# Kernel optimization log

Measured on AMD Instinct MI355X. Metric: run time of the kernel, lower is better.

## Reference

```python
import jax, jax.numpy as jnp
import numpy as np

NEG = -9e15
SLOPE = 0.1  # LeakyReLU negative_slope in the torch module

B, N, NFEAT = 4, 2048, 256
NHID, NHEADS, NOUT = 64, 8, 128


def setup_inputs() -> dict:
    key = jax.random.key(0)
    ks = jax.random.split(key, 8)
    x = jax.random.normal(ks[0], (B, N, NFEAT), dtype=jnp.float32)
    adj = jax.random.randint(ks[1], (B, N, N), 0, 2, dtype=jnp.int32)
    s = 0.1
    Wh = jax.random.normal(ks[2], (NHEADS, NFEAT, NHID), dtype=jnp.float32) * s
    ah = jax.random.normal(ks[3], (NHEADS, 2 * NHID), dtype=jnp.float32) * s
    bh = jax.random.normal(ks[4], (NHEADS, NHID), dtype=jnp.float32) * s
    Wo = jax.random.normal(ks[5], (NHID * NHEADS, NOUT), dtype=jnp.float32) * s
    ao = jax.random.normal(ks[6], (2 * NOUT,), dtype=jnp.float32) * s
    bo = jax.random.normal(ks[7], (NOUT,), dtype=jnp.float32) * s
    return {"x": x, "adj": adj, "Wh": Wh, "ah": ah, "bh": bh,
            "Wo": Wo, "ao": ao, "bo": bo}


def _leaky(v):
    return jnp.where(v >= 0, v, SLOPE * v)


def _gat_layer(x, adj, W, a, b):
    # x: [B,N,Fin], W: [Fin,F], a: [2F], b: [F]
    h = jnp.einsum('bnf,fo->bno', x, W)          # [B,N,F]
    F = W.shape[1]
    a1, a2 = a[:F], a[F:]
    s1 = h @ a1                                   # [B,N] (query / row term)
    s2 = h @ a2                                   # [B,N] (key / col term)
    e = _leaky(s1[:, :, None] + s2[:, None, :])   # [B,N,N], avoids a_input blowup
    e = jnp.where(adj > 0, e, NEG)
    att = jax.nn.softmax(e, axis=2)               # [B,N,N]
    h_prime = jnp.einsum('bnm,bmf->bnf', att, h) + b
    return jax.nn.elu(h_prime)


def reference(x, adj, Wh, ah, bh, Wo, ao, bo):
    # per-head layers, vmapped over the head axis of the stacked params
    heads = jax.vmap(lambda W, a, b: _gat_layer(x, adj, W, a, b))(Wh, ah, bh)
    # [H,B,N,F] -> concat heads along feature dim: [B,N,H*F]
    hcat = jnp.transpose(heads, (1, 2, 0, 3)).reshape(x.shape[0], x.shape[1], -1)
    out = _gat_layer(hcat, adj, Wo, ao, bo)
    return jax.nn.relu(out)
```

## Files before the change

kernel.cpp:

```cpp
#include <hip/hip_runtime.h>

constexpr int B_ = 4;
constexpr int N_ = 2048;
constexpr int NFEAT_ = 256;
constexpr int NHEADS_ = 8;
constexpr float SLOPE_ = 0.1f;
constexpr float L2E = 1.4426950408889634f;

typedef __attribute__((ext_vector_type(8))) __fp16 f16x8;
typedef __attribute__((ext_vector_type(2))) __fp16 f16x2;
typedef __attribute__((ext_vector_type(4))) float f32x4;

__device__ __forceinline__ f16x8 pack8(const float* v) {
  union { f16x2 h2[4]; f16x8 h8; } u;
  u.h2[0] = __builtin_amdgcn_cvt_pkrtz(v[0], v[1]);
  u.h2[1] = __builtin_amdgcn_cvt_pkrtz(v[2], v[3]);
  u.h2[2] = __builtin_amdgcn_cvt_pkrtz(v[4], v[5]);
  u.h2[3] = __builtin_amdgcn_cvt_pkrtz(v[6], v[7]);
  return u.h8;
}

__global__ __launch_bounds__(256) void k_packmask(
    const int* __restrict__ adj, unsigned short* __restrict__ mask2)
{
  const int l = threadIdx.x & 63;
  const size_t gw = ((size_t)blockIdx.x * 256 + threadIdx.x) >> 6;
  const int jt = (int)(gw & 31);
  const int ig16 = (int)((gw >> 5) & 127);
  const int b = (int)(gw >> 12);
  const int q = l >> 4, c15 = l & 15;

  const int* base = adj + ((size_t)b * N_ + ig16 * 16) * N_ + jt * 64 + l;
  unsigned int msk = 0;
  #pragma unroll
  for (int r = 0; r < 16; ++r) {
    int a = base[(size_t)r * N_];
    unsigned long long bal = __ballot(a > 0);
    unsigned int v = (unsigned int)((bal >> (q * 8)) & 0xffull)
                   | ((unsigned int)((bal >> (q * 8 + 32)) & 0xffull) << 8);
    if (r == c15) msk = v;
  }
  mask2[gw * 64 + l] = (unsigned short)msk;
}

__global__ __launch_bounds__(256) void k_rowmax(
    const float* __restrict__ src, float* __restrict__ dst)
{
  int row = blockIdx.x, t = threadIdx.x;
  const float* p = src + (size_t)row * N_;
  float m = -INFINITY;
  #pragma unroll
  for (int k = 0; k < N_ / 256; ++k) m = fmaxf(m, p[t + k * 256]);
  #pragma unroll
  for (int off = 1; off < 64; off <<= 1) m = fmaxf(m, __shfl_xor(m, off, 64));
  __shared__ float sm[4];
  if ((t & 63) == 0) sm[t >> 6] = m;
  __syncthreads();
  if (t == 0) dst[row] = fmaxf(fmaxf(sm[0], sm[1]), fmaxf(sm[2], sm[3]));
}

__global__ __launch_bounds__(256) void k_prepwh(
    const float* __restrict__ Wh, __fp16* __restrict__ WhB)
{
  int l = threadIdx.x & 63;
  int s = (int)((blockIdx.x * 256 + threadIdx.x) >> 6);
  int h = s >> 5, ks = (s >> 2) & 7, ft = s & 3;
  const float* src = Wh + ((size_t)h * 256 + ks * 32 + (l >> 4) * 8) * 64 + ft * 16 + (l & 15);
  float v[8];
  #pragma unroll
  for (int j = 0; j < 8; ++j) v[j] = src[(size_t)j * 64];
  *(f16x8*)(WhB + (size_t)s * 512 + l * 8) = pack8(v);
}

__global__ __launch_bounds__(256) void k_prepwo(
    const float* __restrict__ Wo, __fp16* __restrict__ WoB)
{
  int l = threadIdx.x & 63;
  int s = (int)((blockIdx.x * 256 + threadIdx.x) >> 6);
  int ks = s >> 3, ft = s & 7;
  const float* src = Wo + ((size_t)ks * 32 + (l >> 4) * 8) * 128 + ft * 16 + (l & 15);
  float v[8];
  #pragma unroll
  for (int j = 0; j < 8; ++j) v[j] = src[(size_t)j * 128];
  *(f16x8*)(WoB + (size_t)s * 512 + l * 8) = pack8(v);
}

__global__ __launch_bounds__(256, 4) void k_gemm1(
    const float* __restrict__ x, const __fp16* __restrict__ WhB,
    const float* __restrict__ ah,
    __fp16* __restrict__ hB1, float* __restrict__ s1h, float* __restrict__ s2h)
{
  constexpr int XP = 264;
  __shared__ __fp16 xs[16 * XP];
  __shared__ __fp16 hT[512 * 16];

  const int t = threadIdx.x;
  const int bid = blockIdx.x;
  const int b = bid >> 7;
  const int n0 = (bid & 127) * 16;

  {
    int r = t >> 4, k0 = (t & 15) * 16;
    const float* src = x + ((size_t)(b * N_) + n0 + r) * NFEAT_ + k0;
    float v0[8], v1[8];
    *(float4*)&v0[0] = *(const float4*)(src);
    *(float4*)&v0[4] = *(const float4*)(src + 4);
    *(float4*)&v1[0] = *(const float4*)(src + 8);
    *(float4*)&v1[4] = *(const float4*)(src + 12);
    *(f16x8*)&xs[r * XP + k0] = pack8(v0);
    *(f16x8*)&xs[r * XP + k0 + 8] = pack8(v1);
  }
  __syncthreads();

  const int w = t >> 6, l = t & 63;
  const int quad = l >> 4, c15 = l & 15;

  f32x4 acc[8];
  #pragma unroll
  for (int i = 0; i < 8; ++i) acc[i] = (f32x4){0.f, 0.f, 0.f, 0.f};

  for (int ks = 0; ks < 8; ++ks) {
    f16x8 af = *(const f16x8*)&xs[c15 * XP + ks * 32 + quad * 8];
    #pragma unroll
    for (int tt = 0; tt < 8; ++tt) {
      int hl = tt >> 2, ft = tt & 3;
      f16x8 bf = *(const f16x8*)(WhB +
          ((((size_t)(2 * w + hl) * 8 + ks) * 4 + ft) * 512) + l * 8);
      acc[tt] = __builtin_amdgcn_mfma_f32_16x16x32_f16(af, bf, acc[tt], 0, 0, 0);
    }
  }

  #pragma unroll
  for (int hl = 0; hl < 2; ++hl) {
    int head = 2 * w + hl;
    float a1v[4], a2v[4];
    #pragma unroll
    for (int ft = 0; ft < 4; ++ft) {
      a1v[ft] = ah[head * 128 + ft * 16 + c15] * L2E;
      a2v[ft] = ah[head * 128 + 64 + ft * 16 + c15] * L2E;
    }
    #pragma unroll
    for (int r = 0; r < 4; ++r) {
      float v1 = 0.f, v2 = 0.f;
      #pragma unroll
      for (int ft = 0; ft < 4; ++ft) {
        v1 = fmaf(acc[hl * 4 + ft][r], a1v[ft], v1);
        v2 = fmaf(acc[hl * 4 + ft][r], a2v[ft], v2);
      }
      #pragma unroll
      for (int off = 1; off < 16; off <<= 1) {
        v1 += __shfl_xor(v1, off, 64);
        v2 += __shfl_xor(v2, off, 64);
      }
      if (c15 == 0) {
        s1h[(size_t)(b * NHEADS_ + head) * N_ + n0 + quad * 4 + r] = v1;
        s2h[(size_t)(b * NHEADS_ + head) * N_ + n0 + quad * 4 + r] = v2;
      }
    }
  }

  #pragma unroll
  for (int tt = 0; tt < 8; ++tt) {
    int f = (2 * w + (tt >> 2)) * 64 + (tt & 3) * 16 + c15;
    #pragma unroll
    for (int r = 0; r < 4; ++r)
      hT[f * 16 + quad * 4 + r] = (__fp16)acc[tt][r];
  }
  __syncthreads();

  const int base_oct = (n0 >> 3) & 3;
  #pragma unroll
  for (int q = 0; q < 4; ++q) {
    int s = t + q * 256;
    int c15v = s & 15, oct = (s >> 4) & 1, ft = (s >> 5) & 3, head = s >> 7;
    f16x8 v = *(const f16x8*)&hT[(head * 64 + ft * 16 + c15v) * 16 + oct * 8];
    int lane0 = (base_oct + oct) * 16 + c15v;
    *(f16x8*)(hB1 +
        ((((size_t)(b * NHEADS_ + head) * 64 + (n0 >> 5)) * 4 + ft) * 512) + lane0 * 8) = v;
  }
}

__global__ __launch_bounds__(256, 4) void k_gemm2(
    const __fp16* __restrict__ g1, const __fp16* __restrict__ WoB,
    const float* __restrict__ ao,
    __fp16* __restrict__ hB2, float* __restrict__ s1o, float* __restrict__ s2o)
{
  constexpr int GP = 520;
  __shared__ __fp16 gs[16 * GP];
  __shared__ __fp16 hT[128 * 16];
  __shared__ float sd1[4][16], sd2[4][16];

  const int t = threadIdx.x;
  const int bid = blockIdx.x;
  const int b = bid >> 7;
  const int n0 = (bid & 127) * 16;

  {
    int r = t >> 4, k0 = (t & 15) * 32;
    const __fp16* src = g1 + ((size_t)(b * N_) + n0 + r) * 512 + k0;
    #pragma unroll
    for (int i = 0; i < 4; ++i)
      *(f16x8*)&gs[r * GP + k0 + i * 8] = *(const f16x8*)(src + i * 8);
  }
  __syncthreads();

  const int w = t >> 6, l = t & 63;
  const int quad = l >> 4, c15 = l & 15;

  f32x4 acc[2];
  acc[0] = (f32x4){0.f, 0.f, 0.f, 0.f};
  acc[1] = (f32x4){0.f, 0.f, 0.f, 0.f};

  for (int ks = 0; ks < 16; ++ks) {
    f16x8 af = *(const f16x8*)&gs[c15 * GP + ks * 32 + quad * 8];
    #pragma unroll
    for (int tt = 0; tt < 2; ++tt) {
      int ft = 2 * w + tt;
      f16x8 bf = *(const f16x8*)(WoB + (((size_t)ks * 8 + ft) * 512) + l * 8);
      acc[tt] = __builtin_amdgcn_mfma_f32_16x16x32_f16(af, bf, acc[tt], 0, 0, 0);
    }
  }

  {
    float a1v[2], a2v[2];
    #pragma unroll
    for (int tt = 0; tt < 2; ++tt) {
      int f = (2 * w + tt) * 16 + c15;
      a1v[tt] = ao[f] * L2E;
      a2v[tt] = ao[128 + f] * L2E;
    }
    #pragma unroll
    for (int r = 0; r < 4; ++r) {
      float v1 = acc[0][r] * a1v[0] + acc[1][r] * a1v[1];
      float v2 = acc[0][r] * a2v[0] + acc[1][r] * a2v[1];
      #pragma unroll
      for (int off = 1; off < 16; off <<= 1) {
        v1 += __shfl_xor(v1, off, 64);
        v2 += __shfl_xor(v2, off, 64);
      }
      if (c15 == 0) { sd1[w][quad * 4 + r] = v1; sd2[w][quad * 4 + r] = v2; }
    }
  }

  #pragma unroll
  for (int tt = 0; tt < 2; ++tt) {
    int f = (2 * w + tt) * 16 + c15;
    #pragma unroll
    for (int r = 0; r < 4; ++r)
      hT[f * 16 + quad * 4 + r] = (__fp16)acc[tt][r];
  }
  __syncthreads();

  if (t < 16)
    s1o[(size_t)b * N_ + n0 + t] = sd1[0][t] + sd1[1][t] + sd1[2][t] + sd1[3][t];
  else if (t < 32) {
    int rr = t - 16;
    s2o[(size_t)b * N_ + n0 + rr] = sd2[0][rr] + sd2[1][rr] + sd2[2][rr] + sd2[3][rr];
  }

  {
    int c15v = t & 15, oct = (t >> 4) & 1, ft = t >> 5;
    f16x8 v = *(const f16x8*)&hT[(ft * 16 + c15v) * 16 + oct * 8];
    int base_oct = (n0 >> 3) & 3;
    int lane0 = (base_oct + oct) * 16 + c15v;
    *(f16x8*)(hB2 +
        (((size_t)(b * 64 + (n0 >> 5)) * 8 + ft) * 512) + lane0 * 8) = v;
  }
}

template<int EPI>
__global__ __launch_bounds__(512, 4) void k_att(
    const __fp16* __restrict__ hB, const float* __restrict__ s1,
    const float* __restrict__ s2, const float* __restrict__ s2max,
    const unsigned short* __restrict__ mask2,
    const float* __restrict__ bias, void* __restrict__ outp)
{
  constexpr int H    = (EPI == 0) ? 8 : 1;
  constexpr int NFT  = (EPI == 0) ? 4 : 8;
  constexpr int KSTR = NFT * 512;
  constexpr int OSTR = (EPI == 0) ? 512 : 128;
  constexpr int NRG  = (EPI == 0) ? 4 : 2;
  constexpr int NJQ  = 8 / NRG;
  constexpr int JLEN = N_ / NJQ;
  constexpr int TJ   = (EPI == 0) ? 64 : 32;
  constexpr int NIT  = JLEN / TJ;
  constexpr int IBLK = NRG * 16;
  constexpr int NH   = TJ / 32;
  constexpr int TILE = TJ * 64;
  constexpr int CPT  = (TILE * 2) / (NRG * 64 * 16);

  __shared__ __fp16 vbuf[NJQ][2][TILE];
  __shared__ float s2s[N_];

  const int tid = threadIdx.x;
  const int w = tid >> 6, l = tid & 63;
  const int quad = l >> 4, c15 = l & 15;
  const int rowg = w % NRG, jq = w / NRG;
  const int tc = rowg * 64 + l;

  int idx = blockIdx.x;
  const int ig = idx % (N_ / IBLK); idx /= (N_ / IBLK);
  int head = 0, fs = 0;
  if constexpr (EPI == 0) { head = idx % 8; idx /= 8; }
  else                    { fs = idx % 2; idx /= 2; }
  const int b = idx;

  const int i0w = ig * IBLK + rowg * 16;
  const int colbase = (EPI == 0) ? head * 64 : fs * 64;

  const float* s1p = s1 + (size_t)(b * H + head) * N_;
  const float* s2p = s2 + (size_t)(b * H + head) * N_;
  const char* hBp = (const char*)(hB + (size_t)(b * H + head) * (N_ / 32) * KSTR
                                  + (EPI == 0 ? 0 : fs * 2048));
  const unsigned short* mp = mask2 + ((size_t)(b * 128 + (i0w >> 4)) * 32) * 64 + l;

  *(float4*)&s2s[tid * 4] = *(const float4*)(s2p + tid * 4);

  const float s1v = s1p[i0w + c15];
  const float zm = s1v + s2max[b * H + head];
  const float m = fmaxf(zm, SLOPE_ * zm);
  const float p = s1v - m;
  const float cq = (SLOPE_ - 1.f) * m;

  f16x8 ones;
  #pragma unroll
  for (int i = 0; i < 8; ++i) ones[i] = (__fp16)1.0f;

  f32x4 acc[4], acc5;
  #pragma unroll
  for (int t = 0; t < 4; ++t) acc[t] = (f32x4){0.f, 0.f, 0.f, 0.f};
  acc5 = (f32x4){0.f, 0.f, 0.f, 0.f};

  const int jbase = jq * JLEN;

  auto stage = [&](int j0, int slot) {
    const char* srcb = hBp + (size_t)(j0 >> 5) * (KSTR * 2);
    #pragma unroll
    for (int c = 0; c < CPT; ++c) {
      int off = (tc + c * NRG * 64) * 16;
      const char* g = srcb + off;
      char* d = (char*)&vbuf[jq][slot][0] + (off - l * 16);
      __builtin_amdgcn_global_load_lds(
          (const __attribute__((address_space(1))) unsigned int*)g,
          (__attribute__((address_space(3))) unsigned int*)d, 16, 0, 0);
    }
  };

  stage(jbase, 0);
  unsigned int mk_cur = mp[(size_t)(jbase >> 6) * 64];
  __syncthreads();

  for (int it = 0; it < NIT; ++it) {
    const int cur = it & 1;
    const int j0 = jbase + it * TJ;
    unsigned int mk_next = 0;
    if (it + 1 < NIT) {
      stage(j0 + TJ, cur ^ 1);
      mk_next = mp[(size_t)((j0 + TJ) >> 6) * 64];
    }

    float s2r[NH * 8];
    *(float4*)&s2r[0] = *(const float4*)&s2s[j0 + quad * 8];
    *(float4*)&s2r[4] = *(const float4*)&s2s[j0 + quad * 8 + 4];
    if constexpr (NH == 2) {
      *(float4*)&s2r[8]  = *(const float4*)&s2s[j0 + 32 + quad * 8];
      *(float4*)&s2r[12] = *(const float4*)&s2s[j0 + 32 + quad * 8 + 4];
    }

    f16x8 afr[NH];
    #pragma unroll
    for (int h = 0; h < NH; ++h) {
      unsigned int mbyte;
      if constexpr (EPI == 0) mbyte = (mk_cur >> (h * 8)) & 0xffu;
      else                    mbyte = (mk_cur >> (8 * ((j0 >> 5) & 1))) & 0xffu;
      float wgt[8];
      #pragma unroll
      for (int k = 0; k < 8; ++k) {
        float t0 = p + s2r[h * 8 + k];
        float t1 = fmaf(SLOPE_, t0, cq);
        float tm = fmaxf(t0, t1);
        float e = __builtin_amdgcn_exp2f(tm);
        int sel = (int)(mbyte << (31 - k)) >> 31;
        union { float f; int i; } u; u.f = e; u.i &= sel;
        wgt[k] = u.f;
      }
      afr[h] = pack8(wgt);
    }

    const __fp16* vb = &vbuf[jq][cur][0];
    #pragma unroll
    for (int h = 0; h < NH; ++h) {
      acc5 = __builtin_amdgcn_mfma_f32_16x16x32_f16(afr[h], ones, acc5, 0, 0, 0);
      #pragma unroll
      for (int t = 0; t < 4; ++t) {
        f16x8 bf = *(const f16x8*)(vb + h * 2048 + t * 512 + l * 8);
        acc[t] = __builtin_amdgcn_mfma_f32_16x16x32_f16(afr[h], bf, acc[t], 0, 0, 0);
      }
    }

    mk_cur = mk_next;
    __syncthreads();
  }

  auto pacc = (float(*)[NRG][16][64])(&vbuf[0][0][0]);
  auto pls  = (float(*)[NRG][16])(&s2s[0]);
  if (jq > 0) {
    #pragma unroll
    for (int t = 0; t < 4; ++t)
      #pragma unroll
      for (int r = 0; r < 4; ++r)
        pacc[jq - 1][rowg][quad * 4 + r][t * 16 + c15] = acc[t][r];
    if (c15 == 0) {
      #pragma unroll
      for (int r = 0; r < 4; ++r)
        pls[jq - 1][rowg][quad * 4 + r] = acc5[r];
    }
  }
  __syncthreads();
  if (jq == 0) {
    float Lrow[4];
    #pragma unroll
    for (int r = 0; r < 4; ++r) Lrow[r] = acc5[r];
    #pragma unroll
    for (int q = 0; q < NJQ - 1; ++q) {
      #pragma unroll
      for (int t = 0; t < 4; ++t)
        #pragma unroll
        for (int r = 0; r < 4; ++r)
          acc[t][r] += pacc[q][rowg][quad * 4 + r][t * 16 + c15];
      #pragma unroll
      for (int r = 0; r < 4; ++r) Lrow[r] += pls[q][rowg][quad * 4 + r];
    }
    float lr[4];
    #pragma unroll
    for (int r = 0; r < 4; ++r) lr[r] = 1.f / Lrow[r];

    #pragma unroll
    for (int t = 0; t < 4; ++t) {
      const float bv = bias[colbase + t * 16 + c15];
      #pragma unroll
      for (int r = 0; r < 4; ++r) {
        const int i = i0w + quad * 4 + r;
        float v = acc[t][r] * lr[r] + bv;
        if constexpr (EPI == 0) {
          v = (v > 0.f) ? v : expm1f(v);
          ((__fp16*)outp)[(size_t)(b * N_ + i) * OSTR + colbase + t * 16 + c15] = (__fp16)v;
        } else {
          v = fmaxf(v, 0.f);
          ((float*)outp)[(size_t)(b * N_ + i) * OSTR + colbase + t * 16 + c15] = v;
        }
      }
    }
  }
}

extern "C" void kernel_launch(void* const* d_in, const int* in_sizes, int n_in,
                              void* d_out, int out_size, void* d_ws, size_t ws_size,
                              hipStream_t stream) {
  const float* x   = (const float*)d_in[0];
  const int*   adj = (const int*)d_in[1];
  const float* Wh  = (const float*)d_in[2];
  const float* ah  = (const float*)d_in[3];
  const float* bh  = (const float*)d_in[4];
  const float* Wo  = (const float*)d_in[5];
  const float* ao  = (const float*)d_in[6];
  const float* bo  = (const float*)d_in[7];
  float* out = (float*)d_out;

  float* ws   = (float*)d_ws;
  float* s1h  = ws;
  float* s2h  = s1h  + (size_t)B_ * NHEADS_ * N_;
  float* s1o  = s2h  + (size_t)B_ * NHEADS_ * N_;
  float* s2o  = s1o  + (size_t)B_ * N_;
  float* s2mh = s2o  + (size_t)B_ * N_;
  float* s2mo = s2mh + 64;
  __fp16* g1  = (__fp16*)(s2mo + 64);
  __fp16* hB1 = g1  + (size_t)B_ * N_ * 512;
  __fp16* hB2 = hB1 + (size_t)B_ * NHEADS_ * N_ * 64;
  __fp16* WhB = hB2 + (size_t)B_ * N_ * 128;
  __fp16* WoB = WhB + (size_t)8 * 256 * 64;
  unsigned short* mask2 = (unsigned short*)(WoB + (size_t)512 * 128);

  k_packmask<<<(B_ * 128 * 32 * 64) / 256, 256, 0, stream>>>(adj, mask2);
  k_prepwh<<<64, 256, 0, stream>>>(Wh, WhB);
  k_prepwo<<<32, 256, 0, stream>>>(Wo, WoB);
  k_gemm1<<<B_ * (N_ / 16), 256, 0, stream>>>(x, WhB, ah, hB1, s1h, s2h);
  k_rowmax<<<B_ * NHEADS_, 256, 0, stream>>>(s2h, s2mh);
  k_att<0><<<B_ * NHEADS_ * (N_ / 64), 512, 0, stream>>>(
      hB1, s1h, s2h, s2mh, mask2, bh, (void*)g1);
  k_gemm2<<<B_ * (N_ / 16), 256, 0, stream>>>(g1, WoB, ao, hB2, s1o, s2o);
  k_rowmax<<<B_, 256, 0, stream>>>(s2o, s2mo);
  k_att<1><<<B_ * 2 * (N_ / 32), 512, 0, stream>>>(
      hB2, s1o, s2o, s2mo, mask2, bo, (void*)out);
}
```

Baseline: 208.9 us.

## Merge prep kernels, fold rowmax into attention, retile both attention kernels

Combines the mask-pack and two weight-prep kernels into one launch. Removes the separate row-max kernels by computing the s2 max inside each attention block from the staged s2 vector. Splits the templated attention kernel into two specialised ones: layer 1 uses 128-column j tiles with 2 j-quarters, and layer 2 computes all 128 output features per block instead of splitting features across blocks. The fp16 stores in the GEMMs become packed 4-wide writes. This cuts launch count and redundant logit work, at the cost of larger LDS tiles and more registers per block, which may reduce occupancy.

```diff
diff --git a/kernel.cpp b/kernel.cpp
--- a/kernel.cpp
+++ b/kernel.cpp
@@ -8,6 +8,7 @@
 constexpr float L2E = 1.4426950408889634f;
 
 typedef __attribute__((ext_vector_type(8))) __fp16 f16x8;
+typedef __attribute__((ext_vector_type(4))) __fp16 f16x4;
 typedef __attribute__((ext_vector_type(2))) __fp16 f16x2;
 typedef __attribute__((ext_vector_type(4))) float f32x4;
 
@@ -19,70 +20,54 @@
   u.h2[3] = __builtin_amdgcn_cvt_pkrtz(v[6], v[7]);
   return u.h8;
 }
-
-__global__ __launch_bounds__(256) void k_packmask(
-    const int* __restrict__ adj, unsigned short* __restrict__ mask2)
-{
-  const int l = threadIdx.x & 63;
-  const size_t gw = ((size_t)blockIdx.x * 256 + threadIdx.x) >> 6;
-  const int jt = (int)(gw & 31);
-  const int ig16 = (int)((gw >> 5) & 127);
-  const int b = (int)(gw >> 12);
-  const int q = l >> 4, c15 = l & 15;
-
-  const int* base = adj + ((size_t)b * N_ + ig16 * 16) * N_ + jt * 64 + l;
-  unsigned int msk = 0;
-  #pragma unroll
-  for (int r = 0; r < 16; ++r) {
-    int a = base[(size_t)r * N_];
-    unsigned long long bal = __ballot(a > 0);
-    unsigned int v = (unsigned int)((bal >> (q * 8)) & 0xffull)
-                   | ((unsigned int)((bal >> (q * 8 + 32)) & 0xffull) << 8);
-    if (r == c15) msk = v;
-  }
-  mask2[gw * 64 + l] = (unsigned short)msk;
-}
-
-__global__ __launch_bounds__(256) void k_rowmax(
-    const float* __restrict__ src, float* __restrict__ dst)
-{
-  int row = blockIdx.x, t = threadIdx.x;
-  const float* p = src + (size_t)row * N_;
-  float m = -INFINITY;
-  #pragma unroll
-  for (int k = 0; k < N_ / 256; ++k) m = fmaxf(m, p[t + k * 256]);
-  #pragma unroll
-  for (int off = 1; off < 64; off <<= 1) m = fmaxf(m, __shfl_xor(m, off, 64));
-  __shared__ float sm[4];
-  if ((t & 63) == 0) sm[t >> 6] = m;
-  __syncthreads();
-  if (t == 0) dst[row] = fmaxf(fmaxf(sm[0], sm[1]), fmaxf(sm[2], sm[3]));
-}
-
-__global__ __launch_bounds__(256) void k_prepwh(
-    const float* __restrict__ Wh, __fp16* __restrict__ WhB)
-{
-  int l = threadIdx.x & 63;
-  int s = (int)((blockIdx.x * 256 + threadIdx.x) >> 6);
-  int h = s >> 5, ks = (s >> 2) & 7, ft = s & 3;
-  const float* src = Wh + ((size_t)h * 256 + ks * 32 + (l >> 4) * 8) * 64 + ft * 16 + (l & 15);
-  float v[8];
-  #pragma unroll
-  for (int j = 0; j < 8; ++j) v[j] = src[(size_t)j * 64];
-  *(f16x8*)(WhB + (size_t)s * 512 + l * 8) = pack8(v);
-}
-
-__global__ __launch_bounds__(256) void k_prepwo(
+__device__ __forceinline__ f16x4 pack4(float a, float b, float c, float d) {
+  union { f16x2 h2[2]; f16x4 h4; } u;
+  u.h2[0] = __builtin_amdgcn_cvt_pkrtz(a, b);
+  u.h2[1] = __builtin_amdgcn_cvt_pkrtz(c, d);
+  return u.h4;
+}
+
+__global__ __launch_bounds__(256) void k_prep(
+    const int* __restrict__ adj, unsigned short* __restrict__ mask2,
+    const float* __restrict__ Wh, __fp16* __restrict__ WhB,
     const float* __restrict__ Wo, __fp16* __restrict__ WoB)
 {
-  int l = threadIdx.x & 63;
-  int s = (int)((blockIdx.x * 256 + threadIdx.x) >> 6);
-  int ks = s >> 3, ft = s & 7;
-  const float* src = Wo + ((size_t)ks * 32 + (l >> 4) * 8) * 128 + ft * 16 + (l & 15);
-  float v[8];
-  #pragma unroll
-  for (int j = 0; j < 8; ++j) v[j] = src[(size_t)j * 128];
-  *(f16x8*)(WoB + (size_t)s * 512 + l * 8) = pack8(v);
+  const int bid = blockIdx.x;
+  const int l = threadIdx.x & 63;
+  if (bid < 4096) {
+    const size_t gw = ((size_t)bid * 256 + threadIdx.x) >> 6;
+    const int jt = (int)(gw & 31);
+    const int ig16 = (int)((gw >> 5) & 127);
+    const int b = (int)(gw >> 12);
+    const int q = l >> 4, c15 = l & 15;
+    const int* base = adj + ((size_t)b * N_ + ig16 * 16) * N_ + jt * 64 + l;
+    unsigned int msk = 0;
+    #pragma unroll
+    for (int r = 0; r < 16; ++r) {
+      int a = base[(size_t)r * N_];
+      unsigned long long bal = __ballot(a > 0);
+      unsigned int v = (unsigned int)((bal >> (q * 8)) & 0xffull)
+                     | ((unsigned int)((bal >> (q * 8 + 32)) & 0xffull) << 8);
+      if (r == c15) msk = v;
+    }
+    mask2[gw * 64 + l] = (unsigned short)msk;
+  } else if (bid < 4160) {
+    int s = (int)(((bid - 4096) * 256 + threadIdx.x) >> 6);
+    int h = s >> 5, ks = (s >> 2) & 7, ft = s & 3;
+    const float* src = Wh + ((size_t)h * 256 + ks * 32 + (l >> 4) * 8) * 64 + ft * 16 + (l & 15);
+    float v[8];
+    #pragma unroll
+    for (int j = 0; j < 8; ++j) v[j] = src[(size_t)j * 64];
+    *(f16x8*)(WhB + (size_t)s * 512 + l * 8) = pack8(v);
+  } else {
+    int s = (int)(((bid - 4160) * 256 + threadIdx.x) >> 6);
+    int ks = s >> 3, ft = s & 7;
+    const float* src = Wo + ((size_t)ks * 32 + (l >> 4) * 8) * 128 + ft * 16 + (l & 15);
+    float v[8];
+    #pragma unroll
+    for (int j = 0; j < 8; ++j) v[j] = src[(size_t)j * 128];
+    *(f16x8*)(WoB + (size_t)s * 512 + l * 8) = pack8(v);
+  }
 }
 
 __global__ __launch_bounds__(256, 4) void k_gemm1(
@@ -162,9 +147,8 @@
   #pragma unroll
   for (int tt = 0; tt < 8; ++tt) {
     int f = (2 * w + (tt >> 2)) * 64 + (tt & 3) * 16 + c15;
-    #pragma unroll
-    for (int r = 0; r < 4; ++r)
-      hT[f * 16 + quad * 4 + r] = (__fp16)acc[tt][r];
+    *(f16x4*)&hT[f * 16 + quad * 4] =
+        pack4(acc[tt][0], acc[tt][1], acc[tt][2], acc[tt][3]);
   }
   __syncthreads();
 
@@ -245,9 +229,8 @@
   #pragma unroll
   for (int tt = 0; tt < 2; ++tt) {
     int f = (2 * w + tt) * 16 + c15;
-    #pragma unroll
-    for (int r = 0; r < 4; ++r)
-      hT[f * 16 + quad * 4 + r] = (__fp16)acc[tt][r];
+    *(f16x4*)&hT[f * 16 + quad * 4] =
+        pack4(acc[tt][0], acc[tt][1], acc[tt][2], acc[tt][3]);
   }
   __syncthreads();
 
@@ -268,29 +251,17 @@
   }
 }
 
-template<int EPI>
-__global__ __launch_bounds__(512, 4) void k_att(
+__global__ __launch_bounds__(512, 4) void k_att1(
     const __fp16* __restrict__ hB, const float* __restrict__ s1,
-    const float* __restrict__ s2, const float* __restrict__ s2max,
-    const unsigned short* __restrict__ mask2,
-    const float* __restrict__ bias, void* __restrict__ outp)
+    const float* __restrict__ s2, const unsigned short* __restrict__ mask2,
+    const float* __restrict__ bias, __fp16* __restrict__ g1)
 {
-  constexpr int H    = (EPI == 0) ? 8 : 1;
-  constexpr int NFT  = (EPI == 0) ? 4 : 8;
-  constexpr int KSTR = NFT * 512;
-  constexpr int OSTR = (EPI == 0) ? 512 : 128;
-  constexpr int NRG  = (EPI == 0) ? 4 : 2;
-  constexpr int NJQ  = 8 / NRG;
-  constexpr int JLEN = N_ / NJQ;
-  constexpr int TJ   = (EPI == 0) ? 64 : 32;
-  constexpr int NIT  = JLEN / TJ;
-  constexpr int IBLK = NRG * 16;
-  constexpr int NH   = TJ / 32;
+  constexpr int NRG = 4, NJQ = 2, JLEN = 1024, TJ = 128, NIT = JLEN / TJ;
   constexpr int TILE = TJ * 64;
-  constexpr int CPT  = (TILE * 2) / (NRG * 64 * 16);
 
   __shared__ __fp16 vbuf[NJQ][2][TILE];
   __shared__ float s2s[N_];
+  __shared__ float red[8];
 
   const int tid = threadIdx.x;
   const int w = tid >> 6, l = tid & 63;
@@ -299,25 +270,47 @@
   const int tc = rowg * 64 + l;
 
   int idx = blockIdx.x;
-  const int ig = idx % (N_ / IBLK); idx /= (N_ / IBLK);
-  int head = 0, fs = 0;
-  if constexpr (EPI == 0) { head = idx % 8; idx /= 8; }
-  else                    { fs = idx % 2; idx /= 2; }
-  const int b = idx;
-
-  const int i0w = ig * IBLK + rowg * 16;
-  const int colbase = (EPI == 0) ? head * 64 : fs * 64;
-
-  const float* s1p = s1 + (size_t)(b * H + head) * N_;
-  const float* s2p = s2 + (size_t)(b * H + head) * N_;
-  const char* hBp = (const char*)(hB + (size_t)(b * H + head) * (N_ / 32) * KSTR
-                                  + (EPI == 0 ? 0 : fs * 2048));
+  const int ig = idx & 31; idx >>= 5;
+  const int head = idx & 7;
+  const int b = idx >> 3;
+  const int i0w = ig * 64 + rowg * 16;
+
+  const float* s1p = s1 + (size_t)(b * 8 + head) * N_;
+  const float* s2p = s2 + (size_t)(b * 8 + head) * N_;
+  const char* hBp = (const char*)(hB + (size_t)(b * 8 + head) * (N_ / 32) * 2048);
   const unsigned short* mp = mask2 + ((size_t)(b * 128 + (i0w >> 4)) * 32) * 64 + l;
 
-  *(float4*)&s2s[tid * 4] = *(const float4*)(s2p + tid * 4);
-
+  const int jbase = jq * JLEN;
+
+  auto stage = [&](int j0, int slot) {
+    const char* srcb = hBp + (size_t)(j0 >> 5) * 4096;
+    #pragma unroll
+    for (int c = 0; c < 4; ++c) {
+      int off = (tc + c * 256) * 16;
+      __builtin_amdgcn_global_load_lds(
+          (const __attribute__((address_space(1))) unsigned int*)(srcb + off),
+          (__attribute__((address_space(3))) unsigned int*)
+              ((char*)&vbuf[jq][slot][0] + (off - l * 16)), 16, 0, 0);
+    }
+  };
+
+  stage(jbase, 0);
+  unsigned int mk0 = mp[(size_t)(jbase >> 6) * 64];
+  unsigned int mk1 = mp[(size_t)((jbase >> 6) + 1) * 64];
+
+  float4 sv = *(const float4*)(s2p + tid * 4);
+  *(float4*)&s2s[tid * 4] = sv;
+  float lm = fmaxf(fmaxf(sv.x, sv.y), fmaxf(sv.z, sv.w));
+  #pragma unroll
+  for (int off = 1; off < 64; off <<= 1) lm = fmaxf(lm, __shfl_xor(lm, off, 64));
+  if (l == 0) red[w] = lm;
   const float s1v = s1p[i0w + c15];
-  const float zm = s1v + s2max[b * H + head];
+  __syncthreads();
+  float s2m = red[0];
+  #pragma unroll
+  for (int q = 1; q < 8; ++q) s2m = fmaxf(s2m, red[q]);
+
+  const float zm = s1v + s2m;
   const float m = fmaxf(zm, SLOPE_ * zm);
   const float p = s1v - m;
   const float cq = (SLOPE_ - 1.f) * m;
@@ -331,52 +324,28 @@
   for (int t = 0; t < 4; ++t) acc[t] = (f32x4){0.f, 0.f, 0.f, 0.f};
   acc5 = (f32x4){0.f, 0.f, 0.f, 0.f};
 
-  const int jbase = jq * JLEN;
-
-  auto stage = [&](int j0, int slot) {
-    const char* srcb = hBp + (size_t)(j0 >> 5) * (KSTR * 2);
-    #pragma unroll
-    for (int c = 0; c < CPT; ++c) {
-      int off = (tc + c * NRG * 64) * 16;
-      const char* g = srcb + off;
-      char* d = (char*)&vbuf[jq][slot][0] + (off - l * 16);
-      __builtin_amdgcn_global_load_lds(
-          (const __attribute__((address_space(1))) unsigned int*)g,
-          (__attribute__((address_space(3))) unsigned int*)d, 16, 0, 0);
-    }
-  };
-
-  stage(jbase, 0);
-  unsigned int mk_cur = mp[(size_t)(jbase >> 6) * 64];
-  __syncthreads();
-
   for (int it = 0; it < NIT; ++it) {
     const int cur = it & 1;
     const int j0 = jbase + it * TJ;
-    unsigned int mk_next = 0;
+    unsigned int nk0 = 0, nk1 = 0;
     if (it + 1 < NIT) {
       stage(j0 + TJ, cur ^ 1);
-      mk_next = mp[(size_t)((j0 + TJ) >> 6) * 64];
-    }
-
-    float s2r[NH * 8];
-    *(float4*)&s2r[0] = *(const float4*)&s2s[j0 + quad * 8];
-    *(float4*)&s2r[4] = *(const float4*)&s2s[j0 + quad * 8 + 4];
-    if constexpr (NH == 2) {
-      *(float4*)&s2r[8]  = *(const float4*)&s2s[j0 + 32 + quad * 8];
-      *(float4*)&s2r[12] = *(const float4*)&s2s[j0 + 32 + quad * 8 + 4];
-    }
-
-    f16x8 afr[NH];
-    #pragma unroll
-    for (int h = 0; h < NH; ++h) {
-      unsigned int mbyte;
-      if constexpr (EPI == 0) mbyte = (mk_cur >> (h * 8)) & 0xffu;
-      else                    mbyte = (mk_cur >> (8 * ((j0 >> 5) & 1))) & 0xffu;
+      nk0 = mp[(size_t)((j0 + TJ) >> 6) * 64];
+      nk1 = mp[(size_t)(((j0 + TJ) >> 6) + 1) * 64];
+    }
+
+    #pragma unroll
+    for (int h = 0; h < 4; ++h) {
+      const int jk = j0 + h * 32;
+      float s2r[8];
+      *(float4*)&s2r[0] = *(const float4*)&s2s[jk + quad * 8];
+      *(float4*)&s2r[4] = *(const float4*)&s2s[jk + quad * 8 + 4];
+      const unsigned int mk = (h < 2) ? mk0 : mk1;
+      const unsigned int mbyte = (mk >> (8 * (h & 1))) & 0xffu;
       float wgt[8];
       #pragma unroll
       for (int k = 0; k < 8; ++k) {
-        float t0 = p + s2r[h * 8 + k];
+        float t0 = p + s2r[k];
         float t1 = fmaf(SLOPE_, t0, cq);
         float tm = fmaxf(t0, t1);
         float e = __builtin_amdgcn_exp2f(tm);
@@ -384,36 +353,178 @@
         union { float f; int i; } u; u.f = e; u.i &= sel;
         wgt[k] = u.f;
       }
-      afr[h] = pack8(wgt);
-    }
-
+      f16x8 a = pack8(wgt);
+      acc5 = __builtin_amdgcn_mfma_f32_16x16x32_f16(a, ones, acc5, 0, 0, 0);
+      const __fp16* vb = &vbuf[jq][cur][h * 2048];
+      #pragma unroll
+      for (int t = 0; t < 4; ++t) {
+        f16x8 bf = *(const f16x8*)(vb + t * 512 + l * 8);
+        acc[t] = __builtin_amdgcn_mfma_f32_16x16x32_f16(a, bf, acc[t], 0, 0, 0);
+      }
+    }
+    mk0 = nk0; mk1 = nk1;
+    __syncthreads();
+  }
+
+  auto pacc = (float(*)[16][64])(&vbuf[0][0][0]);
+  auto pls  = (float(*)[16])(&s2s[0]);
+  if (jq == 1) {
+    #pragma unroll
+    for (int t = 0; t < 4; ++t)
+      #pragma unroll
+      for (int r = 0; r < 4; ++r)
+        pacc[rowg][quad * 4 + r][t * 16 + c15] = acc[t][r];
+    if (c15 == 0) {
+      #pragma unroll
+      for (int r = 0; r < 4; ++r) pls[rowg][quad * 4 + r] = acc5[r];
+    }
+  }
+  __syncthreads();
+  if (jq == 0) {
+    float Lrow[4];
+    #pragma unroll
+    for (int r = 0; r < 4; ++r)
+      Lrow[r] = acc5[r] + pls[rowg][quad * 4 + r];
+    #pragma unroll
+    for (int t = 0; t < 4; ++t)
+      #pragma unroll
+      for (int r = 0; r < 4; ++r)
+        acc[t][r] += pacc[rowg][quad * 4 + r][t * 16 + c15];
+    float lr[4];
+    #pragma unroll
+    for (int r = 0; r < 4; ++r) lr[r] = 1.f / Lrow[r];
+    #pragma unroll
+    for (int t = 0; t < 4; ++t) {
+      const float bv = bias[head * 64 + t * 16 + c15];
+      #pragma unroll
+      for (int r = 0; r < 4; ++r) {
+        const int i = i0w + quad * 4 + r;
+        float v = acc[t][r] * lr[r] + bv;
+        v = (v > 0.f) ? v : expm1f(v);
+        g1[(size_t)(b * N_ + i) * 512 + head * 64 + t * 16 + c15] = (__fp16)v;
+      }
+    }
+  }
+}
+
+__global__ __launch_bounds__(512, 2) void k_att2(
+    const __fp16* __restrict__ hB, const float* __restrict__ s1,
+    const float* __restrict__ s2, const unsigned short* __restrict__ mask2,
+    const float* __restrict__ bias, float* __restrict__ out)
+{
+  constexpr int NRG = 2, NJQ = 4, JLEN = 512, TJ = 32, NIT = JLEN / TJ;
+  constexpr int TILE = TJ * 128;
+
+  __shared__ __fp16 vbuf[NJQ][2][TILE];
+  __shared__ float s2s[N_];
+  __shared__ float red[8];
+
+  const int tid = threadIdx.x;
+  const int w = tid >> 6, l = tid & 63;
+  const int quad = l >> 4, c15 = l & 15;
+  const int rowg = w % NRG, jq = w / NRG;
+  const int tc = rowg * 64 + l;
+
+  int idx = blockIdx.x;
+  const int ig = idx & 63;
+  const int b = idx >> 6;
+  const int i0w = ig * 32 + rowg * 16;
+
+  const float* s1p = s1 + (size_t)b * N_;
+  const float* s2p = s2 + (size_t)b * N_;
+  const char* hBp = (const char*)(hB + (size_t)b * 64 * 4096);
+  const unsigned short* mp = mask2 + ((size_t)(b * 128 + (i0w >> 4)) * 32) * 64 + l;
+
+  const int jbase = jq * JLEN;
+
+  auto stage = [&](int j0, int slot) {
+    const char* srcb = hBp + (size_t)(j0 >> 5) * 8192;
+    #pragma unroll
+    for (int c = 0; c < 4; ++c) {
+      int off = (tc + c * 128) * 16;
+      __builtin_amdgcn_global_load_lds(
+          (const __attribute__((address_space(1))) unsigned int*)(srcb + off),
+          (__attribute__((address_space(3))) unsigned int*)
+              ((char*)&vbuf[jq][slot][0] + (off - l * 16)), 16, 0, 0);
+    }
+  };
+
+  stage(jbase, 0);
+  unsigned int mk = mp[(size_t)(jbase >> 6) * 64];
+
+  float4 sv = *(const float4*)(s2p + tid * 4);
+  *(float4*)&s2s[tid * 4] = sv;
+  float lm = fmaxf(fmaxf(sv.x, sv.y), fmaxf(sv.z, sv.w));
+  #pragma unroll
+  for (int off = 1; off < 64; off <<= 1) lm = fmaxf(lm, __shfl_xor(lm, off, 64));
+  if (l == 0) red[w] = lm;
+  const float s1v = s1p[i0w + c15];
+  __syncthreads();
+  float s2m = red[0];
+  #pragma unroll
+  for (int q = 1; q < 8; ++q) s2m = fmaxf(s2m, red[q]);
+
+  const float zm = s1v + s2m;
+  const float m = fmaxf(zm, SLOPE_ * zm);
+  const float p = s1v - m;
+  const float cq = (SLOPE_ - 1.f) * m;
+
+  f16x8 ones;
+  #pragma unroll
+  for (int i = 0; i < 8; ++i) ones[i] = (__fp16)1.0f;
+
+  f32x4 acc[8], acc5;
+  #pragma unroll
+  for (int t = 0; t < 8; ++t) acc[t] = (f32x4){0.f, 0.f, 0.f, 0.f};
+  acc5 = (f32x4){0.f, 0.f, 0.f, 0.f};
+
+  for (int it = 0; it < NIT; ++it) {
+    const int cur = it & 1;
+    const int j0 = jbase + it * TJ;
+    unsigned int nk = 0;
+    if (it + 1 < NIT) {
+      stage(j0 + TJ, cur ^ 1);
+      nk = mp[(size_t)((j0 + TJ) >> 6) * 64];
+    }
+
+    float s2r[8];
+    *(float4*)&s2r[0] = *(const float4*)&s2s[j0 + quad * 8];
+    *(float4*)&s2r[4] = *(const float4*)&s2s[j0 + quad * 8 + 4];
+    const unsigned int mbyte = (mk >> (8 * ((j0 >> 5) & 1))) & 0xffu;
+    float wgt[8];
+    #pragma unroll
+    for (int k = 0; k < 8; ++k) {
+      float t0 = p + s2r[k];
+      float t1 = fmaf(SLOPE_, t0, cq);
+      float tm = fmaxf(t0, t1);
+      float e = __builtin_amdgcn_exp2f(tm);
+      int sel = (int)(mbyte << (31 - k)) >> 31;
+      union { float f; int i; } u; u.f = e; u.i &= sel;
+      wgt[k] = u.f;
+    }
+    f16x8 a = pack8(wgt);
+    acc5 = __builtin_amdgcn_mfma_f32_16x16x32_f16(a, ones, acc5, 0, 0, 0);
     const __fp16* vb = &vbuf[jq][cur][0];
     #pragma unroll
-    for (int h = 0; h < NH; ++h) {
-      acc5 = __builtin_amdgcn_mfma_f32_16x16x32_f16(afr[h], ones, acc5, 0, 0, 0);
-      #pragma unroll
-      for (int t = 0; t < 4; ++t) {
-        f16x8 bf = *(const f16x8*)(vb + h * 2048 + t * 512 + l * 8);
-        acc[t] = __builtin_amdgcn_mfma_f32_16x16x32_f16(afr[h], bf, acc[t], 0, 0, 0);
-      }
-    }
-
-    mk_cur = mk_next;
+    for (int t = 0; t < 8; ++t) {
+      f16x8 bf = *(const f16x8*)(vb + t * 512 + l * 8);
+      acc[t] = __builtin_amdgcn_mfma_f32_16x16x32_f16(a, bf, acc[t], 0, 0, 0);
+    }
+    mk = nk;
     __syncthreads();
   }
 
-  auto pacc = (float(*)[NRG][16][64])(&vbuf[0][0][0]);
+  auto pacc = (float(*)[NRG][16][128])(&vbuf[0][0][0]);
   auto pls  = (float(*)[NRG][16])(&s2s[0]);
   if (jq > 0) {
     #pragma unroll
-    for (int t = 0; t < 4; ++t)
+    for (int t = 0; t < 8; ++t)
       #pragma unroll
       for (int r = 0; r < 4; ++r)
         pacc[jq - 1][rowg][quad * 4 + r][t * 16 + c15] = acc[t][r];
     if (c15 == 0) {
       #pragma unroll
-      for (int r = 0; r < 4; ++r)
-        pls[jq - 1][rowg][quad * 4 + r] = acc5[r];
+      for (int r = 0; r < 4; ++r) pls[jq - 1][rowg][quad * 4 + r] = acc5[r];
     }
   }
   __syncthreads();
@@ -424,7 +535,7 @@
     #pragma unroll
     for (int q = 0; q < NJQ - 1; ++q) {
       #pragma unroll
-      for (int t = 0; t < 4; ++t)
+      for (int t = 0; t < 8; ++t)
         #pragma unroll
         for (int r = 0; r < 4; ++r)
           acc[t][r] += pacc[q][rowg][quad * 4 + r][t * 16 + c15];
@@ -434,21 +545,14 @@
     float lr[4];
     #pragma unroll
     for (int r = 0; r < 4; ++r) lr[r] = 1.f / Lrow[r];
-
-    #pragma unroll
-    for (int t = 0; t < 4; ++t) {
-      const float bv = bias[colbase + t * 16 + c15];
+    #pragma unroll
+    for (int t = 0; t < 8; ++t) {
+      const float bv = bias[t * 16 + c15];
       #pragma unroll
       for (int r = 0; r < 4; ++r) {
         const int i = i0w + quad * 4 + r;
         float v = acc[t][r] * lr[r] + bv;
-        if constexpr (EPI == 0) {
-          v = (v > 0.f) ? v : expm1f(v);
-          ((__fp16*)outp)[(size_t)(b * N_ + i) * OSTR + colbase + t * 16 + c15] = (__fp16)v;
-        } else {
-          v = fmaxf(v, 0.f);
-          ((float*)outp)[(size_t)(b * N_ + i) * OSTR + colbase + t * 16 + c15] = v;
-        }
+        out[(size_t)(b * N_ + i) * 128 + t * 16 + c15] = fmaxf(v, 0.f);
       }
     }
   }
@@ -472,24 +576,18 @@
   float* s2h  = s1h  + (size_t)B_ * NHEADS_ * N_;
   float* s1o  = s2h  + (size_t)B_ * NHEADS_ * N_;
   float* s2o  = s1o  + (size_t)B_ * N_;
-  float* s2mh = s2o  + (size_t)B_ * N_;
-  float* s2mo = s2mh + 64;
-  __fp16* g1  = (__fp16*)(s2mo + 64);
+  __fp16* g1  = (__fp16*)(s2o + (size_t)B_ * N_);
   __fp16* hB1 = g1  + (size_t)B_ * N_ * 512;
   __fp16* hB2 = hB1 + (size_t)B_ * NHEADS_ * N_ * 64;
   __fp16* WhB = hB2 + (size_t)B_ * N_ * 128;
   __fp16* WoB = WhB + (size_t)8 * 256 * 64;
   unsigned short* mask2 = (unsigned short*)(WoB + (size_t)512 * 128);
 
-  k_packmask<<<(B_ * 128 * 32 * 64) / 256, 256, 0, stream>>>(adj, mask2);
-  k_prepwh<<<64, 256, 0, stream>>>(Wh, WhB);
-  k_prepwo<<<32, 256, 0, stream>>>(Wo, WoB);
+  k_prep<<<4192, 256, 0, stream>>>(adj, mask2, Wh, WhB, Wo, WoB);
   k_gemm1<<<B_ * (N_ / 16), 256, 0, stream>>>(x, WhB, ah, hB1, s1h, s2h);
-  k_rowmax<<<B_ * NHEADS_, 256, 0, stream>>>(s2h, s2mh);
-  k_att<0><<<B_ * NHEADS_ * (N_ / 64), 512, 0, stream>>>(
-      hB1, s1h, s2h, s2mh, mask2, bh, (void*)g1);
+  k_att1<<<B_ * NHEADS_ * (N_ / 64), 512, 0, stream>>>(
+      hB1, s1h, s2h, mask2, bh, g1);
   k_gemm2<<<B_ * (N_ / 16), 256, 0, stream>>>(g1, WoB, ao, hB2, s1o, s2o);
-  k_rowmax<<<B_, 256, 0, stream>>>(s2o, s2mo);
-  k_att<1><<<B_ * 2 * (N_ / 32), 512, 0, stream>>>(
-      hB2, s1o, s2o, s2mo, mask2, bo, (void*)out);
-}
+  k_att2<<<B_ * (N_ / 32), 512, 0, stream>>>(
+      hB2, s1o, s2o, mask2, bo, out);
+}
```

Result: faster. 203.1 us (-2.8%).
